# Kernel tuning notes

Hardware: AMD Instinct MI355X
Metric: run time of the kernel (lower is better)

Reference implementation:

```python
import jax, jax.numpy as jnp
import numpy as np

DIM = 1024
N_HEADS = 16
HEAD_DIM = DIM // N_HEADS
B, N, M = 2, 2048, 2048


def setup_inputs() -> dict:
    key = jax.random.key(0)
    ks = jax.random.split(key, 10)
    s = 1.0 / np.sqrt(DIM)
    return {
        "x1": jax.random.normal(ks[0], (B, N, DIM), dtype=jnp.float32),
        "x2": jax.random.normal(ks[1], (B, M, DIM), dtype=jnp.float32),
        "Wq": jax.random.normal(ks[2], (DIM, DIM), dtype=jnp.float32) * s,
        "bq": jnp.zeros((DIM,), dtype=jnp.float32),
        "Wk": jax.random.normal(ks[3], (DIM, DIM), dtype=jnp.float32) * s,
        "bk": jnp.zeros((DIM,), dtype=jnp.float32),
        "Wv": jax.random.normal(ks[4], (DIM, DIM), dtype=jnp.float32) * s,
        "bv": jnp.zeros((DIM,), dtype=jnp.float32),
        "Wo": jax.random.normal(ks[5], (DIM, DIM), dtype=jnp.float32) * s,
        "bo": jnp.zeros((DIM,), dtype=jnp.float32),
    }


def reference(x1, x2, Wq, bq, Wk, bk, Wv, bv, Wo, bo):
    b, n, _ = x1.shape
    m = x2.shape[1]
    # projections (Linear: x @ W^T + b)
    q = x1 @ Wq.T + bq  # [b, n, dim]
    k = x2 @ Wk.T + bk  # [b, m, dim]
    v = x2 @ Wv.T + bv  # [b, m, dim]
    # split heads -> [b, h, seq, head_dim]
    q = q.reshape(b, n, N_HEADS, HEAD_DIM).transpose(0, 2, 1, 3)
    k = k.reshape(b, m, N_HEADS, HEAD_DIM).transpose(0, 2, 1, 3)
    v = v.reshape(b, m, N_HEADS, HEAD_DIM).transpose(0, 2, 1, 3)
    scale = 1.0 / jnp.sqrt(jnp.asarray(HEAD_DIM, dtype=q.dtype))
    scores = jnp.einsum('bhnd,bhmd->bhnm', q, k) * scale  # [b, h, n, m]
    attn = jax.nn.softmax(scores, axis=-1)
    o = jnp.einsum('bhnm,bhmd->bhnd', attn, v)  # [b, h, n, head_dim]
    o = o.transpose(0, 2, 1, 3).reshape(b, n, DIM)  # merge heads
    return o @ Wo.T + bo
```

## Files before the change

### kernel.cpp

```cpp
#include <hip/hip_runtime.h>
#include <stdint.h>

typedef unsigned short u16;
typedef __attribute__((ext_vector_type(4))) float f32x4;
typedef __attribute__((ext_vector_type(8))) __bf16 bf16x8;
typedef __attribute__((ext_vector_type(4))) __bf16 bf16x4;
typedef __attribute__((ext_vector_type(8))) unsigned short u16x8;
typedef __attribute__((ext_vector_type(4))) unsigned short u16x4;

#define DIM_    1024
#define NHEADS_ 16
#define HD_     64
#define BB_     2
#define NN_     2048
#define MM_     2048

#define QSCALE 0.180336884f

__device__ inline u16 f32_to_bf16u(float f) {
  union { float f; uint32_t u; } x; x.f = f;
  uint32_t r = x.u + 0x7FFFu + ((x.u >> 16) & 1u);
  return (u16)(r >> 16);
}

__device__ inline void gload_lds16(const u16* g, u16* l) {
  u16* gnc = const_cast<u16*>(g);
  __builtin_amdgcn_global_load_lds(
      (__attribute__((address_space(1))) void*)gnc,
      (__attribute__((address_space(3))) void*)l, 16, 0, 0);
}

__global__ void cast_all(const float* s0, u16* d0, const float* s1, u16* d1,
                         const float* s2, u16* d2, const float* s3, u16* d3,
                         const float* s4, u16* d4, const float* s5, u16* d5) {
  const float* s; u16* d; int n4;
  switch (blockIdx.y) {
    case 0: s = s0; d = d0; n4 = (BB_ * NN_ * DIM_) / 4; break;
    case 1: s = s1; d = d1; n4 = (BB_ * MM_ * DIM_) / 4; break;
    case 2: s = s2; d = d2; n4 = (DIM_ * DIM_) / 4; break;
    case 3: s = s3; d = d3; n4 = (DIM_ * DIM_) / 4; break;
    case 4: s = s4; d = d4; n4 = (DIM_ * DIM_) / 4; break;
    default: s = s5; d = d5; n4 = (DIM_ * DIM_) / 4; break;
  }
  int stride = gridDim.x * blockDim.x;
  for (int i = blockIdx.x * blockDim.x + threadIdx.x; i < n4; i += stride) {
    float4 f = reinterpret_cast<const float4*>(s)[i];
    u16x4 u;
    u.x = f32_to_bf16u(f.x);
    u.y = f32_to_bf16u(f.y);
    u.z = f32_to_bf16u(f.z);
    u.w = f32_to_bf16u(f.w);
    reinterpret_cast<u16x4*>(d)[i] = u;
  }
}

#define BM 128
#define BN 128
#define BK 64

template <bool BF16OUT>
__device__ __forceinline__
void gemm_body(const u16* __restrict__ A, const u16* __restrict__ Bm,
               const float* __restrict__ bias, void* __restrict__ Cout,
               int M, int N, int K, float scale,
               u16* As , u16* Bs ) {
  const int tid  = threadIdx.x;
  const int lane = tid & 63;
  const int wid  = tid >> 6;
  const int wr = wid >> 2, wc = wid & 3;
  const int fr = lane & 15, fq = lane >> 4;
  const int bm = blockIdx.x, bn = blockIdx.y;
  const int lrow = lane >> 3;
  const int scol = (((lane & 7) ^ lrow) * 8);

  f32x4 acc[4][2];
  #pragma unroll
  for (int m = 0; m < 4; ++m)
    #pragma unroll
    for (int n = 0; n < 2; ++n)
      acc[m][n] = f32x4{0.f, 0.f, 0.f, 0.f};

  const int NT = K / BK;

  auto stage = [&](int buf, int t) {
    int k0 = t * BK;
    #pragma unroll
    for (int c = 0; c < 2; ++c) {
      int ch  = wid * 2 + c;
      int row = ch * 8 + lrow;
      gload_lds16(A  + (size_t)(bm * BM + row) * K + k0 + scol, &As[buf * BM * BK + ch * 512]);
      gload_lds16(Bm + (size_t)(bn * BN + row) * K + k0 + scol, &Bs[buf * BN * BK + ch * 512]);
    }
  };

  stage(0, 0);
  __syncthreads();
  int cur = 0;
  for (int t = 0; t < NT; ++t) {
    if (t + 1 < NT) stage(cur ^ 1, t + 1);
    #pragma unroll
    for (int ks = 0; ks < 2; ++ks) {
      bf16x8 af[4], bfr[2];
      #pragma unroll
      for (int m = 0; m < 4; ++m)
        af[m] = *reinterpret_cast<const bf16x8*>(
            &As[cur * BM * BK + (wr * 64 + m * 16 + fr) * BK + (((ks * 4 + fq) ^ (fr & 7)) * 8)]);
      #pragma unroll
      for (int n = 0; n < 2; ++n)
        bfr[n] = *reinterpret_cast<const bf16x8*>(
            &Bs[cur * BN * BK + (wc * 32 + n * 16 + fr) * BK + (((ks * 4 + fq) ^ (fr & 7)) * 8)]);
      __builtin_amdgcn_s_setprio(1);
      #pragma unroll
      for (int m = 0; m < 4; ++m)
        #pragma unroll
        for (int n = 0; n < 2; ++n)
          acc[m][n] = __builtin_amdgcn_mfma_f32_16x16x32_bf16(af[m], bfr[n], acc[m][n], 0, 0, 0);
      __builtin_amdgcn_s_setprio(0);
    }
    __syncthreads();
    cur ^= 1;
  }

  #pragma unroll
  for (int n = 0; n < 2; ++n) {
    int col = bn * BN + wc * 32 + n * 16 + fr;
    float bv = bias[col];
    #pragma unroll
    for (int m = 0; m < 4; ++m) {
      #pragma unroll
      for (int i = 0; i < 4; ++i) {
        int row = bm * BM + wr * 64 + m * 16 + fq * 4 + i;
        float v = (acc[m][n][i] + bv) * scale;
        if (BF16OUT)
          ((u16*)Cout)[(size_t)row * N + col] = f32_to_bf16u(v);
        else
          ((float*)Cout)[(size_t)row * N + col] = v;
      }
    }
  }
}

__global__ __launch_bounds__(512)
void gemm_qkv(const u16* __restrict__ x1b, const u16* __restrict__ x2b,
              const u16* __restrict__ Wqb, const float* __restrict__ bq, u16* qb,
              const u16* __restrict__ Wkb, const float* __restrict__ bk, u16* kb,
              const u16* __restrict__ Wvb, const float* __restrict__ bv, u16* vb) {
  __shared__ __align__(16) u16 As[2 * BM * BK];
  __shared__ __align__(16) u16 Bs[2 * BN * BK];
  const u16* A; const u16* W; const float* bias; u16* C; float scale;
  switch (blockIdx.z) {
    case 0:  A = x1b; W = Wqb; bias = bq; C = qb; scale = QSCALE; break;
    case 1:  A = x2b; W = Wkb; bias = bk; C = kb; scale = 1.0f;   break;
    default: A = x2b; W = Wvb; bias = bv; C = vb; scale = 1.0f;   break;
  }
  gemm_body<true>(A, W, bias, C, BB_ * NN_, DIM_, DIM_, scale, As, Bs);
}

__global__ __launch_bounds__(512)
void gemm_o(const u16* __restrict__ A, const u16* __restrict__ W,
            const float* __restrict__ bias, float* __restrict__ C) {
  __shared__ __align__(16) u16 As[2 * BM * BK];
  __shared__ __align__(16) u16 Bs[2 * BN * BK];
  gemm_body<false>(A, W, bias, C, BB_ * NN_, DIM_, DIM_, 1.0f, As, Bs);
}

#define QB 128
#define KVB 64

__global__ __launch_bounds__(512)
void attn_fwd(const u16* __restrict__ qg, const u16* __restrict__ kg,
              const u16* __restrict__ vg, u16* __restrict__ og) {
  __shared__ __align__(16) u16 Ks[4][KVB * HD_];
  __shared__ __align__(16) u16 VTs[4][HD_ * KVB];
  __shared__ __align__(16) u16 Ps[8][16 * KVB];
  const int tid = threadIdx.x, lane = tid & 63, wid = tid >> 6;
  const int fr = lane & 15, fq = lane >> 4;

  int lin = blockIdx.x + gridDim.x * (blockIdx.y + gridDim.y * blockIdx.z);
  int xcd = lin & 7, slot = lin >> 3;
  int r = slot & 15, gg = slot >> 4;
  int g = xcd + 8 * gg;
  int h = g & 15, b = g >> 4;

  const int q0 = r * QB + wid * 16;
  const size_t base_q  = (size_t)b * NN_ * DIM_ + (size_t)h * HD_;
  const size_t base_kv = (size_t)b * MM_ * DIM_ + (size_t)h * HD_;
  const int lrow = lane >> 3;
  const int scol = (((lane & 7) ^ lrow) * 8);
  const int ksw = (fr & 7);
  const int psw = (fr & 7) ^ (fr >> 3);

  bf16x8 qf[2];
  #pragma unroll
  for (int ks = 0; ks < 2; ++ks)
    qf[ks] = *reinterpret_cast<const bf16x8*>(qg + base_q + (size_t)(q0 + fr) * DIM_ + ks * 32 + fq * 8);

  bf16x8 onesf;
  #pragma unroll
  for (int j = 0; j < 8; ++j) onesf[j] = (__bf16)1.0f;

  f32x4 oacc[4];
  #pragma unroll
  for (int db = 0; db < 4; ++db) oacc[db] = f32x4{0.f, 0.f, 0.f, 0.f};
  f32x4 lacc = f32x4{0.f, 0.f, 0.f, 0.f};

  const int NT = MM_ / KVB;

  auto stageK = [&](int buf, int t) {
    int kv0 = t * KVB;
    int row = wid * 8 + lrow;
    gload_lds16(kg + base_kv + (size_t)(kv0 + row) * DIM_ + scol, &Ks[buf][wid * 512]);
  };
  auto loadV = [&](int t, u16x8& vpre) {
    int kv0 = t * KVB;
    vpre = *reinterpret_cast<const u16x8*>(vg + base_kv + (size_t)(kv0 + lane) * DIM_ + wid * 8);
  };
  auto writeVT = [&](int buf, const u16x8& vpre) {
    #pragma unroll
    for (int j = 0; j < 8; ++j)
      VTs[buf][(wid * 8 + j) * KVB + (((lane >> 3) ^ j) * 8) + (lane & 7)] = vpre[j];
  };

  u16* Pw = Ps[wid];

  auto compute = [&](int buf) {
    f32x4 s[4];
    #pragma unroll
    for (int nb = 0; nb < 4; ++nb) s[nb] = f32x4{0.f, 0.f, 0.f, 0.f};
    __builtin_amdgcn_s_setprio(1);
    #pragma unroll
    for (int nb = 0; nb < 4; ++nb)
      #pragma unroll
      for (int ks = 0; ks < 2; ++ks) {
        bf16x8 kf = *reinterpret_cast<const bf16x8*>(
            &Ks[buf][(nb * 16 + fr) * HD_ + (((ks * 4 + fq) ^ ksw) * 8)]);
        s[nb] = __builtin_amdgcn_mfma_f32_16x16x32_bf16(kf, qf[ks], s[nb], 0, 0, 0);
      }
    __builtin_amdgcn_s_setprio(0);

    #pragma unroll
    for (int nb = 0; nb < 4; ++nb) {
      bf16x4 pk;
      #pragma unroll
      for (int i = 0; i < 4; ++i)
        pk[i] = (__bf16)__builtin_amdgcn_exp2f(s[nb][i]);
      *reinterpret_cast<bf16x4*>(
          &Pw[fr * KVB + (((2 * nb + (fq >> 1)) ^ psw) * 8) + (fq & 1) * 4]) = pk;
    }

    __builtin_amdgcn_s_setprio(1);
    #pragma unroll
    for (int ks = 0; ks < 2; ++ks) {
      bf16x8 pf = *reinterpret_cast<const bf16x8*>(
          &Pw[fr * KVB + (((ks * 4 + fq) ^ psw) * 8)]);
      lacc = __builtin_amdgcn_mfma_f32_16x16x32_bf16(pf, onesf, lacc, 0, 0, 0);
      #pragma unroll
      for (int db = 0; db < 4; ++db) {
        bf16x8 vf = *reinterpret_cast<const bf16x8*>(
            &VTs[buf][(db * 16 + fr) * KVB + (((ks * 4 + fq) ^ ksw) * 8)]);
        oacc[db] = __builtin_amdgcn_mfma_f32_16x16x32_bf16(pf, vf, oacc[db], 0, 0, 0);
      }
    }
    __builtin_amdgcn_s_setprio(0);
  };

  {
    u16x8 v0, v1;
    loadV(0, v0);
    loadV(1, v1);
    stageK(0, 0);
    stageK(1, 1);
    writeVT(0, v0);
    writeVT(1, v1);
    __syncthreads();
  }

  for (int it = 0; it < NT / 2; ++it) {
    int t0 = 2 * it;
    u16x8 vpre0, vpre1;
    bool pre = (t0 + 2 < NT);
    if (pre) {
      loadV(t0 + 2, vpre0);
      loadV(t0 + 3, vpre1);
      stageK((t0 + 2) & 3, t0 + 2);
      stageK((t0 + 3) & 3, t0 + 3);
    }
    compute(t0 & 3);
    compute((t0 + 1) & 3);
    if (pre) {
      writeVT((t0 + 2) & 3, vpre0);
      writeVT((t0 + 3) & 3, vpre1);
    }
    __syncthreads();
  }

  #pragma unroll
  for (int i = 0; i < 4; ++i) {
    float inv = 1.f / lacc[i];
    size_t rowoff = base_q + (size_t)(q0 + fq * 4 + i) * DIM_;
    #pragma unroll
    for (int db = 0; db < 4; ++db)
      og[rowoff + db * 16 + fr] = f32_to_bf16u(oacc[db][i] * inv);
  }
}

extern "C" void kernel_launch(void* const* d_in, const int* in_sizes, int n_in,
                              void* d_out, int out_size, void* d_ws, size_t ws_size,
                              hipStream_t stream) {
  (void)in_sizes; (void)n_in; (void)out_size; (void)ws_size;
  const float* x1 = (const float*)d_in[0];
  const float* x2 = (const float*)d_in[1];
  const float* Wq = (const float*)d_in[2];
  const float* bq = (const float*)d_in[3];
  const float* Wk = (const float*)d_in[4];
  const float* bk = (const float*)d_in[5];
  const float* Wv = (const float*)d_in[6];
  const float* bv = (const float*)d_in[7];
  const float* Wo = (const float*)d_in[8];
  const float* bo = (const float*)d_in[9];
  float* out = (float*)d_out;

  char* ws = (char*)d_ws;
  u16* x1b = (u16*)(ws);
  u16* x2b = (u16*)(ws + (8u  << 20));
  u16* Wqb = (u16*)(ws + (16u << 20));
  u16* Wkb = (u16*)(ws + (18u << 20));
  u16* Wvb = (u16*)(ws + (20u << 20));
  u16* Wob = (u16*)(ws + (22u << 20));
  u16* qb  = (u16*)(ws + (24u << 20));
  u16* kb  = (u16*)(ws + (32u << 20));
  u16* vb  = (u16*)(ws + (40u << 20));
  u16* ob  = (u16*)(ws + (48u << 20));

  cast_all<<<dim3(512, 6), 256, 0, stream>>>(x1, x1b, x2, x2b, Wq, Wqb,
                                             Wk, Wkb, Wv, Wvb, Wo, Wob);

  const int Mrows = BB_ * NN_;
  dim3 gqkv(Mrows / BM, DIM_ / BN, 3);
  gemm_qkv<<<gqkv, 512, 0, stream>>>(x1b, x2b, Wqb, bq, qb, Wkb, bk, kb, Wvb, bv, vb);

  dim3 ga(NN_ / QB, NHEADS_, BB_);
  attn_fwd<<<ga, 512, 0, stream>>>(qb, kb, vb, ob);

  dim3 gg(Mrows / BM, DIM_ / BN);
  gemm_o<<<gg, 512, 0, stream>>>(ob, Wob, bo, out);
}
```

Before: 121.9 us.

## Switch attention to 32x32 MFMA with register-resident P and split-KV waves

Rewrites the attention inner loop to use 32x32x16 bf16 MFMAs, splitting each 64-key tile between wave pairs. The probability tile no longer round-trips through shared memory: it is packed with cvt_pk_bf16 and rearranged across lanes with permlane32_swap. The row sum is now a scalar add in registers instead of an extra MFMA against a ones vector. Partial outputs from the two key-halves are merged through shared memory at the end, and stores are coalesced through an LDS staging buffer; this adds an epilogue sync and reduction.

```diff
diff --git a/kernel.cpp b/kernel.cpp
--- a/kernel.cpp
+++ b/kernel.cpp
@@ -3,8 +3,8 @@
 
 typedef unsigned short u16;
 typedef __attribute__((ext_vector_type(4))) float f32x4;
+typedef __attribute__((ext_vector_type(16))) float f32x16;
 typedef __attribute__((ext_vector_type(8))) __bf16 bf16x8;
-typedef __attribute__((ext_vector_type(4))) __bf16 bf16x4;
 typedef __attribute__((ext_vector_type(8))) unsigned short u16x8;
 typedef __attribute__((ext_vector_type(4))) unsigned short u16x4;
 
@@ -28,6 +28,15 @@
   __builtin_amdgcn_global_load_lds(
       (__attribute__((address_space(1))) void*)gnc,
       (__attribute__((address_space(3))) void*)l, 16, 0, 0);
+}
+
+__device__ inline uint32_t cvt_pk_bf16(float lo, float hi) {
+  uint32_t r;
+  asm("v_cvt_pk_bf16_f32 %0, %1, %2" : "=v"(r) : "v"(lo), "v"(hi));
+  return r;
+}
+__device__ inline void permlane32_swap(uint32_t& a, uint32_t& b) {
+  asm("v_permlane32_swap_b32 %0, %1" : "+v"(a), "+v"(b));
 }
 
 __global__ void cast_all(const float* s0, u16* d0, const float* s1, u16* d1,
@@ -172,37 +181,35 @@
               const u16* __restrict__ vg, u16* __restrict__ og) {
   __shared__ __align__(16) u16 Ks[4][KVB * HD_];
   __shared__ __align__(16) u16 VTs[4][HD_ * KVB];
-  __shared__ __align__(16) u16 Ps[8][16 * KVB];
   const int tid = threadIdx.x, lane = tid & 63, wid = tid >> 6;
-  const int fr = lane & 15, fq = lane >> 4;
+  const int hi = lane >> 5;
+  const int l31 = lane & 31;
+  const int wq = wid >> 1, wk = wid & 1;
 
   int lin = blockIdx.x + gridDim.x * (blockIdx.y + gridDim.y * blockIdx.z);
   int xcd = lin & 7, slot = lin >> 3;
-  int r = slot & 15, gg = slot >> 4;
-  int g = xcd + 8 * gg;
+  int r = slot & 15, gg2 = slot >> 4;
+  int g = xcd + 8 * gg2;
   int h = g & 15, b = g >> 4;
 
-  const int q0 = r * QB + wid * 16;
   const size_t base_q  = (size_t)b * NN_ * DIM_ + (size_t)h * HD_;
   const size_t base_kv = (size_t)b * MM_ * DIM_ + (size_t)h * HD_;
   const int lrow = lane >> 3;
   const int scol = (((lane & 7) ^ lrow) * 8);
-  const int ksw = (fr & 7);
-  const int psw = (fr & 7) ^ (fr >> 3);
-
-  bf16x8 qf[2];
-  #pragma unroll
-  for (int ks = 0; ks < 2; ++ks)
-    qf[ks] = *reinterpret_cast<const bf16x8*>(qg + base_q + (size_t)(q0 + fr) * DIM_ + ks * 32 + fq * 8);
-
-  bf16x8 onesf;
-  #pragma unroll
-  for (int j = 0; j < 8; ++j) onesf[j] = (__bf16)1.0f;
-
-  f32x4 oacc[4];
-  #pragma unroll
-  for (int db = 0; db < 4; ++db) oacc[db] = f32x4{0.f, 0.f, 0.f, 0.f};
-  f32x4 lacc = f32x4{0.f, 0.f, 0.f, 0.f};
+
+  bf16x8 qf[4];
+  const int qrow = r * QB + wq * 32 + l31;
+  #pragma unroll
+  for (int step = 0; step < 4; ++step)
+    qf[step] = *reinterpret_cast<const bf16x8*>(
+        qg + base_q + (size_t)qrow * DIM_ + step * 16 + hi * 8);
+
+  f32x16 oacc[2];
+  #pragma unroll
+  for (int dgrp = 0; dgrp < 2; ++dgrp)
+    #pragma unroll
+    for (int rg = 0; rg < 16; ++rg) oacc[dgrp][rg] = 0.f;
+  float l_run = 0.f;
 
   const int NT = MM_ / KVB;
 
@@ -221,46 +228,51 @@
       VTs[buf][(wid * 8 + j) * KVB + (((lane >> 3) ^ j) * 8) + (lane & 7)] = vpre[j];
   };
 
-  u16* Pw = Ps[wid];
+  union PB { uint32_t w[4]; bf16x8 v; };
 
   auto compute = [&](int buf) {
-    f32x4 s[4];
-    #pragma unroll
-    for (int nb = 0; nb < 4; ++nb) s[nb] = f32x4{0.f, 0.f, 0.f, 0.f};
+    f32x16 s;
+    #pragma unroll
+    for (int rg = 0; rg < 16; ++rg) s[rg] = 0.f;
     __builtin_amdgcn_s_setprio(1);
     #pragma unroll
-    for (int nb = 0; nb < 4; ++nb)
-      #pragma unroll
-      for (int ks = 0; ks < 2; ++ks) {
-        bf16x8 kf = *reinterpret_cast<const bf16x8*>(
-            &Ks[buf][(nb * 16 + fr) * HD_ + (((ks * 4 + fq) ^ ksw) * 8)]);
-        s[nb] = __builtin_amdgcn_mfma_f32_16x16x32_bf16(kf, qf[ks], s[nb], 0, 0, 0);
-      }
+    for (int step = 0; step < 4; ++step) {
+      bf16x8 kf = *reinterpret_cast<const bf16x8*>(
+          (const char*)&Ks[buf][0] + (wk * 32 + l31) * 128 + (((step * 2 + hi) ^ (lane & 7)) * 16));
+      s = __builtin_amdgcn_mfma_f32_32x32x16_bf16(kf, qf[step], s, 0, 0, 0);
+    }
     __builtin_amdgcn_s_setprio(0);
 
-    #pragma unroll
-    for (int nb = 0; nb < 4; ++nb) {
-      bf16x4 pk;
-      #pragma unroll
-      for (int i = 0; i < 4; ++i)
-        pk[i] = (__bf16)__builtin_amdgcn_exp2f(s[nb][i]);
-      *reinterpret_cast<bf16x4*>(
-          &Pw[fr * KVB + (((2 * nb + (fq >> 1)) ^ psw) * 8) + (fq & 1) * 4]) = pk;
+    float p[16];
+    #pragma unroll
+    for (int rg = 0; rg < 16; ++rg) p[rg] = __builtin_amdgcn_exp2f(s[rg]);
+    float lp = 0.f;
+    #pragma unroll
+    for (int rg = 0; rg < 16; ++rg) lp += p[rg];
+    l_run += lp;
+
+    PB pb[2];
+    #pragma unroll
+    for (int u = 0; u < 2; ++u) {
+      uint32_t x0 = cvt_pk_bf16(p[u * 8 + 0], p[u * 8 + 1]);
+      uint32_t y0 = cvt_pk_bf16(p[u * 8 + 4], p[u * 8 + 5]);
+      permlane32_swap(x0, y0);
+      uint32_t x1 = cvt_pk_bf16(p[u * 8 + 2], p[u * 8 + 3]);
+      uint32_t y1 = cvt_pk_bf16(p[u * 8 + 6], p[u * 8 + 7]);
+      permlane32_swap(x1, y1);
+      pb[u].w[0] = x0; pb[u].w[1] = x1; pb[u].w[2] = y0; pb[u].w[3] = y1;
     }
 
     __builtin_amdgcn_s_setprio(1);
     #pragma unroll
-    for (int ks = 0; ks < 2; ++ks) {
-      bf16x8 pf = *reinterpret_cast<const bf16x8*>(
-          &Pw[fr * KVB + (((ks * 4 + fq) ^ psw) * 8)]);
-      lacc = __builtin_amdgcn_mfma_f32_16x16x32_bf16(pf, onesf, lacc, 0, 0, 0);
-      #pragma unroll
-      for (int db = 0; db < 4; ++db) {
+    for (int dgrp = 0; dgrp < 2; ++dgrp)
+      #pragma unroll
+      for (int u = 0; u < 2; ++u) {
         bf16x8 vf = *reinterpret_cast<const bf16x8*>(
-            &VTs[buf][(db * 16 + fr) * KVB + (((ks * 4 + fq) ^ ksw) * 8)]);
-        oacc[db] = __builtin_amdgcn_mfma_f32_16x16x32_bf16(pf, vf, oacc[db], 0, 0, 0);
-      }
-    }
+            (const char*)&VTs[buf][0] + (dgrp * 32 + l31) * 128 +
+            (((wk * 4 + u * 2 + hi) ^ (lane & 7)) * 16));
+        oacc[dgrp] = __builtin_amdgcn_mfma_f32_32x32x16_bf16(vf, pb[u].v, oacc[dgrp], 0, 0, 0);
+      }
     __builtin_amdgcn_s_setprio(0);
   };
 
@@ -294,13 +306,48 @@
     __syncthreads();
   }
 
-  #pragma unroll
-  for (int i = 0; i < 4; ++i) {
-    float inv = 1.f / lacc[i];
-    size_t rowoff = base_q + (size_t)(q0 + fq * 4 + i) * DIM_;
-    #pragma unroll
-    for (int db = 0; db < 4; ++db)
-      og[rowoff + db * 16 + fr] = f32_to_bf16u(oacc[db][i] * inv);
+  float* Od = (float*)&Ks[0][0];
+  float* Ls = (float*)&VTs[0][0];
+  u16*  Of  = (u16*)((char*)&VTs[0][0] + 1024);
+
+  if (wk == 1) {
+    #pragma unroll
+    for (int dgrp = 0; dgrp < 2; ++dgrp)
+      #pragma unroll
+      for (int rg = 0; rg < 16; ++rg) {
+        int d = dgrp * 32 + (rg & 3) + 8 * (rg >> 2) + 4 * hi;
+        Od[(wq * 32 + l31) * 64 + d] = oacc[dgrp][rg];
+      }
+    Ls[wq * 64 + hi * 32 + l31] = l_run;
+  }
+  __syncthreads();
+  if (wk == 0) {
+    #pragma unroll
+    for (int dgrp = 0; dgrp < 2; ++dgrp)
+      #pragma unroll
+      for (int rg = 0; rg < 16; ++rg) {
+        int d = dgrp * 32 + (rg & 3) + 8 * (rg >> 2) + 4 * hi;
+        oacc[dgrp][rg] += Od[(wq * 32 + l31) * 64 + d];
+      }
+    float lown = l_run + __shfl_xor(l_run, 32, 64);
+    float lfull = lown + Ls[wq * 64 + l31] + Ls[wq * 64 + 32 + l31];
+    float inv = 1.f / lfull;
+    #pragma unroll
+    for (int dgrp = 0; dgrp < 2; ++dgrp)
+      #pragma unroll
+      for (int rg = 0; rg < 16; ++rg) {
+        int d = dgrp * 32 + (rg & 3) + 8 * (rg >> 2) + 4 * hi;
+        Of[(wq * 32 + l31) * 64 + d] = f32_to_bf16u(oacc[dgrp][rg] * inv);
+      }
+  }
+  __syncthreads();
+  #pragma unroll
+  for (int itr = 0; itr < 2; ++itr) {
+    int idx = itr * 512 + tid;
+    int qq = idx >> 3;
+    int ck = idx & 7;
+    u16x8 v = *reinterpret_cast<const u16x8*>(&Of[qq * 64 + ck * 8]);
+    *reinterpret_cast<u16x8*>(og + base_q + (size_t)(r * QB + qq) * DIM_ + ck * 8) = v;
   }
 }
 
```

Measured after the change: 125.3 us. 1.03x slower.
